# Optimization experiments

Measured on AMD Instinct MI355X. Metric: run time of the kernel, lower is better.

The kernel has to match this reference:

```python
import jax, jax.numpy as jnp
import numpy as np

GAMMA = 0.01
EPS = 0.01

def setup_inputs() -> dict:
    key = jax.random.key(0)
    k1, k2, k3 = jax.random.split(key, 3)
    B, T, IND, WIDTH = 512, 512, 64, 128
    x = jax.random.normal(k1, (B, T, IND), dtype=jnp.float32)
    init_state = jnp.zeros((1, B, WIDTH), dtype=jnp.float32)
    # xavier-uniform-like init for W and V
    lim_w = float(np.sqrt(6.0 / (WIDTH + WIDTH)))
    lim_v = float(np.sqrt(6.0 / (IND + WIDTH)))
    W = jax.random.uniform(k2, (WIDTH, WIDTH), jnp.float32, -lim_w, lim_w)
    V = jax.random.uniform(k3, (IND, WIDTH), jnp.float32, -lim_v, lim_v)
    b = jnp.zeros((WIDTH,), dtype=jnp.float32)
    return {"x": x, "init_state": init_state, "W": W, "V": V, "b": b}

def reference(x, init_state, W, V, b):
    # x: [B, T, ind]; init_state: [1, B, width]
    A = W - W.T  # antisymmetric matrix, computed once
    xV = jnp.einsum('bti,iw->btw', x, V) + b  # precompute input projection

    def step(state, u):
        # state: [B, width]; u: [B, width] (projected input at timestep t)
        new_state = state + EPS * jnp.tanh(state @ A - GAMMA * state + u)
        return new_state, new_state

    state0 = init_state[0]
    final_state, outputs = jax.lax.scan(step, state0, jnp.swapaxes(xV, 0, 1))
    outputs = jnp.swapaxes(outputs, 0, 1)  # [B, T, width]
    return outputs, final_state
```

## Files before the change

kernel.cpp:

```cpp
#include <hip/hip_runtime.h>
#include <hip/hip_bf16.h>

#define B_DIM 512
#define T_DIM 512
#define IND 64
#define WIDTH 128
#define GAMMA 0.01f
#define EPS 0.01f

#define PJ_ROWS 16
#define PJ_NT ((B_DIM * T_DIM) / PJ_ROWS)

__global__ __launch_bounds__(256) void proj_kernel(
    const float* __restrict__ x, const float* __restrict__ V,
    const float* __restrict__ bias, float* __restrict__ out) {
  __shared__ __align__(16) float xs[PJ_ROWS * IND];

  const int tid = threadIdx.x;
  const int c2 = (tid & 63) * 2;
  const int rh = tid >> 6;

  float2 Vreg[IND];
#pragma unroll
  for (int k = 0; k < IND; ++k)
    Vreg[k] = *(const float2*)(V + k * WIDTH + c2);
  const float2 bb = *(const float2*)(bias + c2);

  for (int tile = blockIdx.x; tile < PJ_NT; tile += gridDim.x) {
    const size_t m0 = (size_t)tile * PJ_ROWS;
    __syncthreads();
#pragma unroll
    for (int q = 0; q < 4; ++q)
      xs[tid + 256 * q] = x[m0 * IND + tid + 256 * q];
    __syncthreads();

    float2 acc0 = bb, acc1 = bb, acc2 = bb, acc3 = bb;
#pragma unroll
    for (int k4 = 0; k4 < IND / 4; ++k4) {
      float4 xv0 = ((const float4*)&xs[(rh + 0) * IND])[k4];
      float4 xv1 = ((const float4*)&xs[(rh + 4) * IND])[k4];
      float4 xv2 = ((const float4*)&xs[(rh + 8) * IND])[k4];
      float4 xv3 = ((const float4*)&xs[(rh + 12) * IND])[k4];
#pragma unroll
      for (int j = 0; j < 4; ++j) {
        float2 v = Vreg[4 * k4 + j];
        float e0 = (j == 0) ? xv0.x : (j == 1) ? xv0.y : (j == 2) ? xv0.z : xv0.w;
        float e1 = (j == 0) ? xv1.x : (j == 1) ? xv1.y : (j == 2) ? xv1.z : xv1.w;
        float e2 = (j == 0) ? xv2.x : (j == 1) ? xv2.y : (j == 2) ? xv2.z : xv2.w;
        float e3 = (j == 0) ? xv3.x : (j == 1) ? xv3.y : (j == 2) ? xv3.z : xv3.w;
        acc0.x += e0 * v.x; acc0.y += e0 * v.y;
        acc1.x += e1 * v.x; acc1.y += e1 * v.y;
        acc2.x += e2 * v.x; acc2.y += e2 * v.y;
        acc3.x += e3 * v.x; acc3.y += e3 * v.y;
      }
    }
    *(float2*)(out + (m0 + rh + 0) * WIDTH + c2) = acc0;
    *(float2*)(out + (m0 + rh + 4) * WIDTH + c2) = acc1;
    *(float2*)(out + (m0 + rh + 8) * WIDTH + c2) = acc2;
    *(float2*)(out + (m0 + rh + 12) * WIDTH + c2) = acc3;
  }
}

#define LDS_BARRIER() asm volatile("s_waitcnt lgkmcnt(0)\n\ts_barrier" ::: "memory")

template <int CTRL>
__device__ __forceinline__ float dpp_mov(float x) {
  return __int_as_float(
      __builtin_amdgcn_update_dpp(0, __float_as_int(x), CTRL, 0xf, 0xf, true));
}

__global__ __launch_bounds__(256) void rnn_kernel(
    const float* __restrict__ W, const float* __restrict__ init,
    float* __restrict__ out, float* __restrict__ finals) {
  __shared__ __align__(16) float sL[2][WIDTH];
  const int b = blockIdx.x;
  const int tid = threadIdx.x;
  const int kc = tid & 3;
  const int cp = tid >> 2;
  const int c0 = 2 * cp;

  float Areg[2][32];
  {
    const int k0 = kc * 32;
#pragma unroll
    for (int j = 0; j < 8; ++j) {
      const int ri = (j + 2 * kc) & 7;
      const int k = k0 + ri * 4;
#pragma unroll
      for (int col = 0; col < 2; ++col) {
        const int cc = c0 + col;
        float4 wr = *(const float4*)(W + (size_t)cc * WIDTH + k);
        Areg[col][4 * j + 0] = W[(size_t)(k + 0) * WIDTH + cc] - wr.x;
        Areg[col][4 * j + 1] = W[(size_t)(k + 1) * WIDTH + cc] - wr.y;
        Areg[col][4 * j + 2] = W[(size_t)(k + 2) * WIDTH + cc] - wr.z;
        Areg[col][4 * j + 3] = W[(size_t)(k + 3) * WIDTH + cc] - wr.w;
      }
    }
  }

  float2 s = *(const float2*)(init + (size_t)b * WIDTH + c0);
  if (kc == 0) *(float2*)&sL[0][c0] = s;
  __syncthreads();

  float* outc = out + (size_t)b * T_DIM * WIDTH + c0;
  float2 u0 = *(const float2*)(outc);
  float2 u1 = *(const float2*)(outc + WIDTH);

#pragma unroll 1
  for (int t = 0; t < T_DIM; ++t) {
    const int p = t & 1;
    const float2 u = u0;
    u0 = u1;
    if (t + 2 < T_DIM) u1 = *(const float2*)(outc + (size_t)(t + 2) * WIDTH);

    const float4* sp = (const float4*)&sL[p][0];
    float a00 = 0.f, a01 = 0.f, a10 = 0.f, a11 = 0.f;
#pragma unroll
    for (int j = 0; j < 8; ++j) {
      const int ri = (j + 2 * kc) & 7;
      float4 sv = sp[kc * 8 + ri];
      a00 += sv.x * Areg[0][4 * j + 0];
      a01 += sv.y * Areg[0][4 * j + 1];
      a00 += sv.z * Areg[0][4 * j + 2];
      a01 += sv.w * Areg[0][4 * j + 3];
      a10 += sv.x * Areg[1][4 * j + 0];
      a11 += sv.y * Areg[1][4 * j + 1];
      a10 += sv.z * Areg[1][4 * j + 2];
      a11 += sv.w * Areg[1][4 * j + 3];
    }
    float d0 = a00 + a01;
    float d1 = a10 + a11;
    d0 += dpp_mov<0xB1>(d0);
    d1 += dpp_mov<0xB1>(d1);
    d0 += dpp_mov<0x4E>(d0);
    d1 += dpp_mov<0x4E>(d1);

    const float f0 = d0 - GAMMA * s.x + u.x;
    const float f1 = d1 - GAMMA * s.y + u.y;
    const float e0 = __expf(2.0f * f0);
    const float e1 = __expf(2.0f * f1);
    const float th0 = fmaf(-2.0f, __builtin_amdgcn_rcpf(e0 + 1.0f), 1.0f);
    const float th1 = fmaf(-2.0f, __builtin_amdgcn_rcpf(e1 + 1.0f), 1.0f);
    s.x = fmaf(EPS, th0, s.x);
    s.y = fmaf(EPS, th1, s.y);

    if (kc == 0) {
      *(float2*)(outc + (size_t)t * WIDTH) = s;
      *(float2*)&sL[p ^ 1][c0] = s;
    }
    LDS_BARRIER();
  }

  if (kc == 0) *(float2*)(finals + (size_t)b * WIDTH + c0) = s;
}

extern "C" void kernel_launch(void* const* d_in, const int* in_sizes, int n_in,
                              void* d_out, int out_size, void* d_ws,
                              size_t ws_size, hipStream_t stream) {
  const float* x = (const float*)d_in[0];
  const float* init = (const float*)d_in[1];
  const float* W = (const float*)d_in[2];
  const float* V = (const float*)d_in[3];
  const float* bias = (const float*)d_in[4];

  float* out = (float*)d_out;
  float* finals = out + (size_t)B_DIM * T_DIM * WIDTH;

  proj_kernel<<<2048, 256, 0, stream>>>(x, V, bias, out);
  rnn_kernel<<<B_DIM, 256, 0, stream>>>(W, init, out, finals);
}
```

Measured before the change: 305.7 us.

## Run recurrence with one wavefront per batch row using packed FMAs

Restructures the recurrent kernel so a single 64-lane wavefront handles each batch row. Each lane holds two full columns of the antisymmetric matrix in registers, with the gamma term folded into the diagonal. The per-step cross-wave barrier, the double-buffered LDS state and the DPP reductions go away, and the dot product uses packed two-wide FMAs. The aim is to cut per-timestep synchronization and reduction latency on the serial dependency chain. In exchange each lane does a longer serial FMA chain, reads far more from LDS per step, and needs roughly 256 VGPRs just for the matrix, which risks spills or lower occupancy.

Measured after the change: 747.1 us. 144% more time.

```diff
diff --git a/kernel.cpp b/kernel.cpp
--- a/kernel.cpp
+++ b/kernel.cpp
@@ -61,46 +61,30 @@
   }
 }
 
-#define LDS_BARRIER() asm volatile("s_waitcnt lgkmcnt(0)\n\ts_barrier" ::: "memory")
+typedef __attribute__((ext_vector_type(2))) float f32x2;
 
-template <int CTRL>
-__device__ __forceinline__ float dpp_mov(float x) {
-  return __int_as_float(
-      __builtin_amdgcn_update_dpp(0, __float_as_int(x), CTRL, 0xf, 0xf, true));
-}
-
-__global__ __launch_bounds__(256) void rnn_kernel(
+__global__ __launch_bounds__(64) void rnn_kernel(
     const float* __restrict__ W, const float* __restrict__ init,
     float* __restrict__ out, float* __restrict__ finals) {
-  __shared__ __align__(16) float sL[2][WIDTH];
+  __shared__ __align__(16) float sL[WIDTH];
   const int b = blockIdx.x;
-  const int tid = threadIdx.x;
-  const int kc = tid & 3;
-  const int cp = tid >> 2;
-  const int c0 = 2 * cp;
+  const int lane = threadIdx.x;
+  const int c0 = 2 * lane;
 
-  float Areg[2][32];
-  {
-    const int k0 = kc * 32;
+  f32x2 Areg[WIDTH];
 #pragma unroll
-    for (int j = 0; j < 8; ++j) {
-      const int ri = (j + 2 * kc) & 7;
-      const int k = k0 + ri * 4;
-#pragma unroll
-      for (int col = 0; col < 2; ++col) {
-        const int cc = c0 + col;
-        float4 wr = *(const float4*)(W + (size_t)cc * WIDTH + k);
-        Areg[col][4 * j + 0] = W[(size_t)(k + 0) * WIDTH + cc] - wr.x;
-        Areg[col][4 * j + 1] = W[(size_t)(k + 1) * WIDTH + cc] - wr.y;
-        Areg[col][4 * j + 2] = W[(size_t)(k + 2) * WIDTH + cc] - wr.z;
-        Areg[col][4 * j + 3] = W[(size_t)(k + 3) * WIDTH + cc] - wr.w;
-      }
-    }
+  for (int k = 0; k < WIDTH; ++k) {
+    float2 wr = *(const float2*)(W + (size_t)k * WIDTH + c0);
+    float a0 = wr.x - W[(size_t)c0 * WIDTH + k];
+    float a1 = wr.y - W[(size_t)(c0 + 1) * WIDTH + k];
+    if (k == c0) a0 -= GAMMA;
+    if (k == c0 + 1) a1 -= GAMMA;
+    Areg[k] = (f32x2){a0, a1};
   }
 
-  float2 s = *(const float2*)(init + (size_t)b * WIDTH + c0);
-  if (kc == 0) *(float2*)&sL[0][c0] = s;
-  __syncthreads();
+  float2 s2 = *(const float2*)(init + (size_t)b * WIDTH + c0);
+  f32x2 s = (f32x2){s2.x, s2.y};
+  *(float2*)&sL[c0] = s2;
 
   float* outc = out + (size_t)b * T_DIM * WIDTH + c0;
   float2 u0 = *(const float2*)(outc);
@@ -108,35 +92,26 @@
 
 #pragma unroll 1
   for (int t = 0; t < T_DIM; ++t) {
-    const int p = t & 1;
     const float2 u = u0;
     u0 = u1;
-    if (t + 2 < T_DIM) u1 = *(const float2*)(outc + (size_t)(t + 2) * WIDTH);
+    const int tp = (t + 2 < T_DIM) ? t + 2 : T_DIM - 1;
+    u1 = *(const float2*)(outc + (size_t)tp * WIDTH);
 
-    const float4* sp = (const float4*)&sL[p][0];
-    float a00 = 0.f, a01 = 0.f, a10 = 0.f, a11 = 0.f;
+    const float4* sp = (const float4*)sL;
+    f32x2 acc0 = {0.f, 0.f}, acc1 = {0.f, 0.f};
+    f32x2 acc2 = {0.f, 0.f}, acc3 = {0.f, 0.f};
 #pragma unroll
-    for (int j = 0; j < 8; ++j) {
-      const int ri = (j + 2 * kc) & 7;
-      float4 sv = sp[kc * 8 + ri];
-      a00 += sv.x * Areg[0][4 * j + 0];
-      a01 += sv.y * Areg[0][4 * j + 1];
-      a00 += sv.z * Areg[0][4 * j + 2];
-      a01 += sv.w * Areg[0][4 * j + 3];
-      a10 += sv.x * Areg[1][4 * j + 0];
-      a11 += sv.y * Areg[1][4 * j + 1];
-      a10 += sv.z * Areg[1][4 * j + 2];
-      a11 += sv.w * Areg[1][4 * j + 3];
+    for (int k4 = 0; k4 < WIDTH / 4; ++k4) {
+      float4 sv = sp[k4];
+      acc0 = __builtin_elementwise_fma((f32x2){sv.x, sv.x}, Areg[4 * k4 + 0], acc0);
+      acc1 = __builtin_elementwise_fma((f32x2){sv.y, sv.y}, Areg[4 * k4 + 1], acc1);
+      acc2 = __builtin_elementwise_fma((f32x2){sv.z, sv.z}, Areg[4 * k4 + 2], acc2);
+      acc3 = __builtin_elementwise_fma((f32x2){sv.w, sv.w}, Areg[4 * k4 + 3], acc3);
     }
-    float d0 = a00 + a01;
-    float d1 = a10 + a11;
-    d0 += dpp_mov<0xB1>(d0);
-    d1 += dpp_mov<0xB1>(d1);
-    d0 += dpp_mov<0x4E>(d0);
-    d1 += dpp_mov<0x4E>(d1);
+    f32x2 dot = (acc0 + acc1) + (acc2 + acc3);
 
-    const float f0 = d0 - GAMMA * s.x + u.x;
-    const float f1 = d1 - GAMMA * s.y + u.y;
+    const float f0 = dot.x + u.x;
+    const float f1 = dot.y + u.y;
     const float e0 = __expf(2.0f * f0);
     const float e1 = __expf(2.0f * f1);
     const float th0 = fmaf(-2.0f, __builtin_amdgcn_rcpf(e0 + 1.0f), 1.0f);
@@ -144,14 +119,12 @@
     s.x = fmaf(EPS, th0, s.x);
     s.y = fmaf(EPS, th1, s.y);
 
-    if (kc == 0) {
-      *(float2*)(outc + (size_t)t * WIDTH) = s;
-      *(float2*)&sL[p ^ 1][c0] = s;
-    }
-    LDS_BARRIER();
+    const float2 ns = make_float2(s.x, s.y);
+    *(float2*)(outc + (size_t)t * WIDTH) = ns;
+    *(float2*)&sL[c0] = ns;
   }
 
-  if (kc == 0) *(float2*)(finals + (size_t)b * WIDTH + c0) = s;
+  *(float2*)(finals + (size_t)b * WIDTH + c0) = make_float2(s.x, s.y);
 }
 
 extern "C" void kernel_launch(void* const* d_in, const int* in_sizes, int n_in,
@@ -167,5 +140,5 @@
   float* finals = out + (size_t)B_DIM * T_DIM * WIDTH;
 
   proj_kernel<<<2048, 256, 0, stream>>>(x, V, bias, out);
-  rnn_kernel<<<B_DIM, 256, 0, stream>>>(W, init, out, finals);
+  rnn_kernel<<<B_DIM, 64, 0, stream>>>(W, init, out, finals);
 }
```
